# Kernel tuning notes

Hardware: AMD Instinct MI355X
Metric: run time of the kernel (lower is better)

## Reference

```python
import jax, jax.numpy as jnp
import numpy as np

NUM_HEADS = 32
MAX_BIAS_LENGTH = 1024
ROPE_BASE = 10000.0


def _rope_cos_sin(seq_len, head_dim, dtype):
    half = head_dim // 2
    inv_freq = 1.0 / (ROPE_BASE ** (jnp.arange(0, half, dtype=jnp.float32) / half))
    t = jnp.arange(seq_len, dtype=jnp.float32)
    freqs = jnp.outer(t, inv_freq)  # [S, half]
    return jnp.cos(freqs).astype(dtype), jnp.sin(freqs).astype(dtype)


def _apply_rope(x, cos, sin):
    # x: [B, S, H, D]; non-interleaved (GPT-NeoX / flash-attn style) rotary
    half = x.shape[-1] // 2
    x1, x2 = x[..., :half], x[..., half:]
    c = cos[None, :, None, :]
    s = sin[None, :, None, :]
    return jnp.concatenate([x1 * c - x2 * s, x1 * s + x2 * c], axis=-1)


def setup_inputs() -> dict:
    key = jax.random.key(0)
    ks = jax.random.split(key, 7)
    B, S, Dm = 2, 2048, 2048
    std = 1.0 / np.sqrt(Dm)
    return {
        "hidden_states": jax.random.normal(ks[0], (B, S, Dm), jnp.float32),
        "Wq": jax.random.normal(ks[1], (Dm, Dm), jnp.float32) * std,
        "Wk": jax.random.normal(ks[2], (Dm, Dm), jnp.float32) * std,
        "Wv": jax.random.normal(ks[3], (Dm, Dm), jnp.float32) * std,
        "Wo": jax.random.normal(ks[4], (Dm, Dm), jnp.float32) * std,
        "learnable_bias": jax.random.normal(ks[5], (NUM_HEADS, MAX_BIAS_LENGTH), jnp.float32) * 0.001,
        "softmax_offset": jnp.zeros((NUM_HEADS,), jnp.float32),
    }


def reference(hidden_states, Wq, Wk, Wv, Wo, learnable_bias, softmax_offset):
    B, S, Dm = hidden_states.shape
    H = NUM_HEADS
    D = Dm // H
    scale = D ** -0.5

    # projections (nn.Linear: x @ W.T)
    q = (hidden_states @ Wq.T).reshape(B, S, H, D)
    k = (hidden_states @ Wk.T).reshape(B, S, H, D)
    v = (hidden_states @ Wv.T).reshape(B, S, H, D)

    cos, sin = _rope_cos_sin(S, D, q.dtype)
    q = _apply_rope(q, cos, sin)
    k = _apply_rope(k, cos, sin)

    q = q.transpose(0, 2, 1, 3)  # [B, H, S, D]
    k = k.transpose(0, 2, 1, 3)
    v = v.transpose(0, 2, 1, 3)

    scores = jnp.einsum("bhid,bhjd->bhij", q, k) * scale  # [B, H, S, S]

    # per-diagonal learnable bias: diag = i - j in [0, MAX_BIAS_LENGTH)
    i = jnp.arange(S)[:, None]
    j = jnp.arange(S)[None, :]
    diag = i - j  # [S, S]
    causal = diag >= 0
    in_band = causal & (diag < MAX_BIAS_LENGTH)
    bias = jnp.where(in_band, learnable_bias[:, jnp.clip(diag, 0, MAX_BIAS_LENGTH - 1)], 0.0)  # [H, S, S]
    scores = scores + bias[None]
    scores = jnp.where(causal[None, None], scores, -jnp.inf)

    # softmax with learnable per-head offset (attention-sink logit)
    off = softmax_offset[None, :, None]  # [1, H, 1]
    m = jnp.maximum(jnp.max(scores, axis=-1), off)  # [B, H, S]
    p = jnp.exp(scores - m[..., None])
    denom = jnp.sum(p, axis=-1) + jnp.exp(off - m)  # [B, H, S]
    out = jnp.einsum("bhij,bhjd->bhid", p, v) / denom[..., None]

    out = out.transpose(0, 2, 1, 3).reshape(B, S, Dm)
    return out @ Wo.T
```

## Files before the change

kernel.cpp:

```cpp
#include <hip/hip_runtime.h>
#include <hip/hip_bf16.h>
#include <stdint.h>

typedef __bf16 bf16x8 __attribute__((ext_vector_type(8)));
typedef float f32x4 __attribute__((ext_vector_type(4)));
typedef unsigned short u16;
typedef u16 u16x4 __attribute__((ext_vector_type(4)));

#define S_LEN 2048
#define DMODEL 2048
#define NHEADS 32
#define BATCH 2
#define MROWS (BATCH * S_LEN)
#define BIAS_LEN 1024
#define LOG2E 1.44269504088896f

__device__ __forceinline__ u16 b16(float f) {
  union { __bf16 h; u16 u; } cv; cv.h = (__bf16)f; return cv.u;
}

__device__ __forceinline__ void gload16(const void* g, void* l) {
  __builtin_amdgcn_global_load_lds(
      (const __attribute__((address_space(1))) uint32_t*)g,
      (__attribute__((address_space(3))) uint32_t*)l, 16, 0, 0);
}

__global__ __launch_bounds__(256)
void cvt_bf16(const float* __restrict__ in, u16* __restrict__ out, int n) {
  int i = (blockIdx.x * 256 + threadIdx.x) * 4;
  if (i >= n) return;
  float4 v = *(const float4*)(in + i);
  u16x4 o = { b16(v.x), b16(v.y), b16(v.z), b16(v.w) };
  *(u16x4*)(out + i) = o;
}

__global__ __launch_bounds__(256)
void rope_tab(float* __restrict__ ct, float* __restrict__ st) {
  int idx = blockIdx.x * 256 + threadIdx.x;
  if (idx >= S_LEN * 32) return;
  int s = idx >> 5, d = idx & 31;
  float inv = exp2f((float)d * (-13.287712379549449f / 32.0f));
  float a = (float)s * inv;
  ct[idx] = cosf(a);
  st[idx] = sinf(a);
}

template<int EPI>
__global__ __launch_bounds__(256)
void gemm_bt(const u16* __restrict__ A, const u16* __restrict__ Bm,
             void* __restrict__ Cout,
             const float* __restrict__ ctab, const float* __restrict__ stab)
{
  __shared__ u16 sA[128 * 64];
  __shared__ u16 sB[128 * 64];
  const int tid  = threadIdx.x;
  const int lane = tid & 63;
  const int wid  = tid >> 6;
  const int wm   = wid >> 1, wn = wid & 1;
  const int lc   = lane & 15, lr = lane >> 4;
  const int tm   = blockIdx.y * 128;
  const int tn   = blockIdx.x * 128;

  f32x4 acc[4][4] = {};

  const u16* aS[4]; const u16* bS[4];
#pragma unroll
  for (int it = 0; it < 4; ++it) {
    int u = it * 256 + tid;
    int row = u >> 3;
    int ch  = (u & 7) ^ (row & 7);
    aS[it] = A  + (size_t)(tm + row) * DMODEL + ch * 8;
    bS[it] = Bm + (size_t)(tn + row) * DMODEL + ch * 8;
  }

  for (int k0 = 0; k0 < DMODEL; k0 += 64) {
    __syncthreads();
#pragma unroll
    for (int it = 0; it < 4; ++it) {
      int u = it * 256 + tid;
      gload16(aS[it] + k0, (char*)sA + u * 16);
      gload16(bS[it] + k0, (char*)sB + u * 16);
    }
    __syncthreads();
#pragma unroll
    for (int kk = 0; kk < 2; ++kk) {
      bf16x8 af[4], bq[4];
#pragma unroll
      for (int mi = 0; mi < 4; ++mi) {
        int row = wm * 64 + mi * 16 + lc;
        int ch  = (kk * 4 + lr) ^ (row & 7);
        af[mi] = *(const bf16x8*)((const char*)sA + row * 128 + ch * 16);
      }
#pragma unroll
      for (int ni = 0; ni < 4; ++ni) {
        int row = wn * 64 + ni * 16 + lc;
        int ch  = (kk * 4 + lr) ^ (row & 7);
        bq[ni] = *(const bf16x8*)((const char*)sB + row * 128 + ch * 16);
      }
#pragma unroll
      for (int mi = 0; mi < 4; ++mi)
#pragma unroll
        for (int ni = 0; ni < 4; ++ni)
          acc[mi][ni] = __builtin_amdgcn_mfma_f32_16x16x32_bf16(af[mi], bq[ni], acc[mi][ni], 0, 0, 0);
    }
  }

  if constexpr (EPI == 4) {
    float* C = (float*)Cout;
#pragma unroll
    for (int mi = 0; mi < 4; ++mi)
#pragma unroll
      for (int ni = 0; ni < 4; ++ni)
#pragma unroll
        for (int j = 0; j < 4; ++j) {
          int r = tm + wm * 64 + mi * 16 + lr * 4 + j;
          int c = tn + wn * 64 + ni * 16 + lc;
          C[(size_t)r * DMODEL + c] = acc[mi][ni][j];
        }
  } else if constexpr (EPI == 3) {
    u16* C = (u16*)Cout;
#pragma unroll
    for (int mi = 0; mi < 4; ++mi)
#pragma unroll
      for (int ni = 0; ni < 4; ++ni) {
        int col = tn + wn * 64 + ni * 16 + lc;
        int hh = col >> 6, d = col & 63;
        int m0 = tm + wm * 64 + mi * 16 + lr * 4;
        int bb = m0 >> 11, s = m0 & 2047;
        u16x4 v = { b16(acc[mi][ni][0]), b16(acc[mi][ni][1]),
                    b16(acc[mi][ni][2]), b16(acc[mi][ni][3]) };
        *(u16x4*)(C + (((size_t)bb * NHEADS + hh) * 64 + d) * S_LEN + s) = v;
      }
  } else {
    u16* C = (u16*)Cout;
#pragma unroll
    for (int mi = 0; mi < 4; ++mi)
#pragma unroll
      for (int ni = 0; ni < 2; ++ni)
#pragma unroll
        for (int j = 0; j < 4; ++j) {
          int col = tn + wn * 64 + ni * 16 + lc;
          int hh = col >> 6, dl = col & 63;
          int r = tm + wm * 64 + mi * 16 + lr * 4 + j;
          int bb = r >> 11, s = r & 2047;
          float x1 = acc[mi][ni][j], x2 = acc[mi][ni + 2][j];
          float cv = ctab[s * 32 + dl], sv = stab[s * 32 + dl];
          float o1 = x1 * cv - x2 * sv;
          float o2 = x1 * sv + x2 * cv;
          if constexpr (EPI == 1) {
            o1 *= 0.125f * LOG2E; o2 *= 0.125f * LOG2E;
          }
          size_t base = (((size_t)bb * NHEADS + hh) * S_LEN + s) * 64 + dl;
          C[base]      = b16(o1);
          C[base + 32] = b16(o2);
        }
  }
}

__global__ __launch_bounds__(512, 6)
void attn_kernel(const u16* __restrict__ Q, const u16* __restrict__ K,
                 const u16* __restrict__ V, const float* __restrict__ biasg,
                 const float* __restrict__ offg, u16* __restrict__ O)
{
  __shared__ __align__(16) u16 sK[2][64 * 64];
  __shared__ __align__(16) u16 sV[2][64 * 64];
  __shared__ __align__(16) u16 sP[8][16 * 40];
  __shared__ float sBias[BIAS_LEN];

  const int tid = threadIdx.x, lane = tid & 63, wid = tid >> 6;
  const int lc = lane & 15, lr = lane >> 4;

  const int L   = blockIdx.x;
  const int idx = L >> 3;
  const int pi  = idx >> 3;
  const int bh  = (L & 7) + 8 * (idx & 7);
  const int h  = bh & 31;
  const int b  = bh >> 5;
  const int qtA  = 31 - pi;
  const int myQt = (wid < 4) ? qtA : pi;
  const int qw   = myQt * 64 + (wid & 3) * 16;

  for (int i = tid; i < BIAS_LEN; i += 512) sBias[i] = biasg[h * BIAS_LEN + i] * LOG2E;
  const float off = offg[h] * LOG2E;

  const u16* qp = Q + ((size_t)bh * S_LEN + qw + lc) * 64;
  bf16x8 aq0 = *(const bf16x8*)(qp + lr * 8);
  bf16x8 aq1 = *(const bf16x8*)(qp + 32 + lr * 8);

  const int srow = tid >> 3;
  const int sch  = (tid & 7) ^ (srow & 7);
  const u16* kSrc = K + ((size_t)bh * S_LEN + srow) * 64 + sch * 8;
  const u16* vSrc = V + ((size_t)bh * 64 + srow) * S_LEN + sch * 8;

  float m = off, lsum = 1.0f;
  f32x4 o[4] = {};

  gload16(kSrc, (char*)sK[0] + tid * 16);
  gload16(vSrc, (char*)sV[0] + tid * 16);
  __syncthreads();

  for (int t = 0; t <= qtA; ++t) {
    const int cur = t & 1;
    if (t < qtA) {
      gload16(kSrc + (size_t)(t + 1) * 64 * 64, (char*)sK[cur ^ 1] + tid * 16);
      gload16(vSrc + (t + 1) * 64,              (char*)sV[cur ^ 1] + tid * 16);
    }

    if (t <= myQt) {
      const int kt = t * 64;
      f32x4 sc[4];
      __builtin_amdgcn_s_setprio(1);
#pragma unroll
      for (int f = 0; f < 4; ++f) {
        int row = f * 16 + lc;
        bf16x8 k0 = *(const bf16x8*)((const char*)sK[cur] + row * 128 + ((lr) ^ (row & 7)) * 16);
        bf16x8 k1 = *(const bf16x8*)((const char*)sK[cur] + row * 128 + ((4 + lr) ^ (row & 7)) * 16);
        f32x4 z = {};
        z     = __builtin_amdgcn_mfma_f32_16x16x32_bf16(k0, aq0, z, 0, 0, 0);
        sc[f] = __builtin_amdgcn_mfma_f32_16x16x32_bf16(k1, aq1, z, 0, 0, 0);
      }
      __builtin_amdgcn_s_setprio(0);

      const int db  = qw + lc - kt;
      const int dqt = qw - kt;
      float pvv[4][4];
      if (t == myQt) {
#pragma unroll
        for (int f = 0; f < 4; ++f)
#pragma unroll
          for (int j = 0; j < 4; ++j) {
            int dd = db - (f * 16 + lr * 4 + j);
            float bb = sBias[dd & 1023];
            pvv[f][j] = (dd >= 0) ? sc[f][j] + bb : -1e30f;
          }
      } else if (dqt <= 1008) {
#pragma unroll
        for (int f = 0; f < 4; ++f)
#pragma unroll
          for (int j = 0; j < 4; ++j)
            pvv[f][j] = sc[f][j] + sBias[db - (f * 16 + lr * 4 + j)];
      } else if (dqt < 1088) {
#pragma unroll
        for (int f = 0; f < 4; ++f)
#pragma unroll
          for (int j = 0; j < 4; ++j) {
            int dd = db - (f * 16 + lr * 4 + j);
            float bb = (dd < 1024) ? sBias[dd & 1023] : 0.0f;
            pvv[f][j] = sc[f][j] + bb;
          }
      } else {
#pragma unroll
        for (int f = 0; f < 4; ++f)
#pragma unroll
          for (int j = 0; j < 4; ++j)
            pvv[f][j] = sc[f][j];
      }

      float pmax = -1e30f;
#pragma unroll
      for (int f = 0; f < 4; ++f) {
        float a = fmaxf(fmaxf(pvv[f][0], pvv[f][1]), fmaxf(pvv[f][2], pvv[f][3]));
        pmax = fmaxf(pmax, a);
      }
      pmax = fmaxf(pmax, __shfl_xor(pmax, 16, 64));
      pmax = fmaxf(pmax, __shfl_xor(pmax, 32, 64));

      if (__any(pmax > m + 8.0f)) {
        float mn = fmaxf(m, pmax);
        float al = exp2f(m - mn);
        m = mn;
        lsum *= al;
        float aj[4];
#pragma unroll
        for (int j = 0; j < 4; ++j) aj[j] = __shfl(al, lr * 4 + j, 64);
#pragma unroll
        for (int f2 = 0; f2 < 4; ++f2)
#pragma unroll
          for (int j = 0; j < 4; ++j) o[f2][j] *= aj[j];
      }

      float rsum = 0.0f;
#pragma unroll
      for (int f = 0; f < 4; ++f)
#pragma unroll
        for (int j = 0; j < 4; ++j) {
          float p = exp2f(pvv[f][j] - m);
          pvv[f][j] = p;
          rsum += p;
        }
      rsum += __shfl_xor(rsum, 16, 64);
      rsum += __shfl_xor(rsum, 32, 64);
      lsum += rsum;

      u16* myP = sP[wid];
#pragma unroll
      for (int kk = 0; kk < 2; ++kk) {
#pragma unroll
        for (int fl = 0; fl < 2; ++fl) {
          int f = kk * 2 + fl;
          u16x4 w = { b16(pvv[f][0]), b16(pvv[f][1]), b16(pvv[f][2]), b16(pvv[f][3]) };
          *(u16x4*)(myP + lc * 40 + fl * 16 + lr * 4) = w;
        }
        asm volatile("s_waitcnt lgkmcnt(0)" ::: "memory");
        __builtin_amdgcn_sched_barrier(0);
        bf16x8 ap = *(const bf16x8*)(myP + lc * 40 + lr * 8);
        __builtin_amdgcn_s_setprio(1);
#pragma unroll
        for (int f2 = 0; f2 < 4; ++f2) {
          int drow = f2 * 16 + lc;
          int chh = (kk * 4 + lr) ^ (drow & 7);
          bf16x8 bv = *(const bf16x8*)((const char*)sV[cur] + drow * 128 + chh * 16);
          o[f2] = __builtin_amdgcn_mfma_f32_16x16x32_bf16(ap, bv, o[f2], 0, 0, 0);
        }
        __builtin_amdgcn_s_setprio(0);
      }
    }
    __syncthreads();
  }

  float ls[4];
#pragma unroll
  for (int j = 0; j < 4; ++j) ls[j] = __shfl(lsum, lr * 4 + j, 64);
#pragma unroll
  for (int f2 = 0; f2 < 4; ++f2)
#pragma unroll
    for (int j = 0; j < 4; ++j) {
      int i = qw + lr * 4 + j;
      int d = f2 * 16 + lc;
      size_t addr = (((size_t)(b * S_LEN + i)) * NHEADS + h) * 64 + d;
      O[addr] = b16(o[f2][j] / ls[j]);
    }
}

extern "C" void kernel_launch(void* const* d_in, const int* in_sizes, int n_in,
                              void* d_out, int out_size, void* d_ws, size_t ws_size,
                              hipStream_t stream)
{
  const float* hs   = (const float*)d_in[0];
  const float* Wq   = (const float*)d_in[1];
  const float* Wk   = (const float*)d_in[2];
  const float* Wv   = (const float*)d_in[3];
  const float* Wo   = (const float*)d_in[4];
  const float* bias = (const float*)d_in[5];
  const float* off  = (const float*)d_in[6];

  char* p = (char*)d_ws;
  u16* hs_b = (u16*)p; p += (size_t)MROWS * DMODEL * 2;
  u16* wq_b = (u16*)p; p += (size_t)DMODEL * DMODEL * 2;
  u16* wk_b = (u16*)p; p += (size_t)DMODEL * DMODEL * 2;
  u16* wv_b = (u16*)p; p += (size_t)DMODEL * DMODEL * 2;
  u16* wo_b = (u16*)p; p += (size_t)DMODEL * DMODEL * 2;
  u16* qf   = (u16*)p; p += (size_t)MROWS * DMODEL * 2;
  u16* kf   = (u16*)p; p += (size_t)MROWS * DMODEL * 2;
  u16* vt   = (u16*)p; p += (size_t)MROWS * DMODEL * 2;
  u16* att  = (u16*)p; p += (size_t)MROWS * DMODEL * 2;
  float* ct = (float*)p; p += (size_t)S_LEN * 32 * 4;
  float* st = (float*)p; p += (size_t)S_LEN * 32 * 4;
  (void)ws_size; (void)in_sizes; (void)n_in; (void)out_size;

  cvt_bf16<<<(MROWS * DMODEL) / 1024, 256, 0, stream>>>(hs, hs_b, MROWS * DMODEL);
  cvt_bf16<<<(DMODEL * DMODEL) / 1024, 256, 0, stream>>>(Wq, wq_b, DMODEL * DMODEL);
  cvt_bf16<<<(DMODEL * DMODEL) / 1024, 256, 0, stream>>>(Wk, wk_b, DMODEL * DMODEL);
  cvt_bf16<<<(DMODEL * DMODEL) / 1024, 256, 0, stream>>>(Wv, wv_b, DMODEL * DMODEL);
  cvt_bf16<<<(DMODEL * DMODEL) / 1024, 256, 0, stream>>>(Wo, wo_b, DMODEL * DMODEL);
  rope_tab<<<(S_LEN * 32) / 256, 256, 0, stream>>>(ct, st);

  dim3 g(DMODEL / 128, MROWS / 128);
  gemm_bt<1><<<g, 256, 0, stream>>>(hs_b, wq_b, qf, ct, st);
  gemm_bt<2><<<g, 256, 0, stream>>>(hs_b, wk_b, kf, ct, st);
  gemm_bt<3><<<g, 256, 0, stream>>>(hs_b, wv_b, vt, nullptr, nullptr);
  attn_kernel<<<dim3(16 * 64), 512, 0, stream>>>(qf, kf, vt, bias, off, att);
  gemm_bt<4><<<g, 256, 0, stream>>>(att, wo_b, d_out, nullptr, nullptr);
}
```

Before: 304.2 us.

## Split paired-tile attention blocks into one-qtile 256-thread blocks with bf16 bias

Each attention block previously handled two query tiles (heavy and light paired) with 512 threads. Now each 256-thread block handles one query tile, launched heaviest-first across twice as many blocks. The bias table is pre-converted to bf16 and scaled by log2e in a new small kernel, which halves its LDS footprint. LDS offsets are precomputed and the final divide becomes a reciprocal multiply. This trades the old balanced pairing for dynamic scheduling, and the bias loses precision from the bf16 rounding.

```diff
diff --git a/kernel.cpp b/kernel.cpp
--- a/kernel.cpp
+++ b/kernel.cpp
@@ -43,6 +43,12 @@
   float a = (float)s * inv;
   ct[idx] = cosf(a);
   st[idx] = sinf(a);
+}
+
+__global__ __launch_bounds__(256)
+void bias_prep(const float* __restrict__ in, u16* __restrict__ out) {
+  int i = blockIdx.x * 256 + threadIdx.x;
+  out[i] = b16(in[i] * LOG2E);
 }
 
 template<int EPI>
@@ -157,170 +163,191 @@
   }
 }
 
-__global__ __launch_bounds__(512, 6)
+__global__ __launch_bounds__(256, 4)
 void attn_kernel(const u16* __restrict__ Q, const u16* __restrict__ K,
-                 const u16* __restrict__ V, const float* __restrict__ biasg,
+                 const u16* __restrict__ V, const u16* __restrict__ bias16,
                  const float* __restrict__ offg, u16* __restrict__ O)
 {
   __shared__ __align__(16) u16 sK[2][64 * 64];
   __shared__ __align__(16) u16 sV[2][64 * 64];
-  __shared__ __align__(16) u16 sP[8][16 * 40];
-  __shared__ float sBias[BIAS_LEN];
+  __shared__ __align__(16) u16 sP[4][16 * 40];
+  __shared__ __align__(8)  u16 sBias[BIAS_LEN];
 
   const int tid = threadIdx.x, lane = tid & 63, wid = tid >> 6;
   const int lc = lane & 15, lr = lane >> 4;
-
-  const int L   = blockIdx.x;
-  const int idx = L >> 3;
-  const int pi  = idx >> 3;
-  const int bh  = (L & 7) + 8 * (idx & 7);
+  const int L  = blockIdx.x;
+  const int qt = 31 - (L >> 6);
+  const int bh = L & 63;
   const int h  = bh & 31;
   const int b  = bh >> 5;
-  const int qtA  = 31 - pi;
-  const int myQt = (wid < 4) ? qtA : pi;
-  const int qw   = myQt * 64 + (wid & 3) * 16;
-
-  for (int i = tid; i < BIAS_LEN; i += 512) sBias[i] = biasg[h * BIAS_LEN + i] * LOG2E;
+  const int qw = qt * 64 + wid * 16;
+
+  *(u16x4*)&sBias[tid * 4] = *(const u16x4*)&bias16[h * BIAS_LEN + tid * 4];
   const float off = offg[h] * LOG2E;
 
   const u16* qp = Q + ((size_t)bh * S_LEN + qw + lc) * 64;
   bf16x8 aq0 = *(const bf16x8*)(qp + lr * 8);
   bf16x8 aq1 = *(const bf16x8*)(qp + 32 + lr * 8);
 
-  const int srow = tid >> 3;
-  const int sch  = (tid & 7) ^ (srow & 7);
-  const u16* kSrc = K + ((size_t)bh * S_LEN + srow) * 64 + sch * 8;
-  const u16* vSrc = V + ((size_t)bh * 64 + srow) * S_LEN + sch * 8;
+  const u16* kS[2]; const u16* vS[2];
+#pragma unroll
+  for (int it = 0; it < 2; ++it) {
+    int u = it * 256 + tid;
+    int row = u >> 3;
+    int ch  = (u & 7) ^ (row & 7);
+    kS[it] = K + ((size_t)bh * S_LEN + row) * 64 + ch * 8;
+    vS[it] = V + ((size_t)bh * 64 + row) * S_LEN + ch * 8;
+  }
+
+  int offK[4][2], offV[2][4];
+#pragma unroll
+  for (int f = 0; f < 4; ++f) {
+    int row = f * 16 + lc;
+    offK[f][0] = row * 128 + ((lr) ^ (row & 7)) * 16;
+    offK[f][1] = row * 128 + ((4 + lr) ^ (row & 7)) * 16;
+  }
+#pragma unroll
+  for (int kk = 0; kk < 2; ++kk)
+#pragma unroll
+    for (int f2 = 0; f2 < 4; ++f2) {
+      int drow = f2 * 16 + lc;
+      offV[kk][f2] = drow * 128 + ((kk * 4 + lr) ^ (drow & 7)) * 16;
+    }
 
   float m = off, lsum = 1.0f;
   f32x4 o[4] = {};
 
-  gload16(kSrc, (char*)sK[0] + tid * 16);
-  gload16(vSrc, (char*)sV[0] + tid * 16);
+#pragma unroll
+  for (int it = 0; it < 2; ++it) {
+    int u = it * 256 + tid;
+    gload16(kS[it], (char*)sK[0] + u * 16);
+    gload16(vS[it], (char*)sV[0] + u * 16);
+  }
   __syncthreads();
 
-  for (int t = 0; t <= qtA; ++t) {
+  for (int t = 0; t <= qt; ++t) {
     const int cur = t & 1;
-    if (t < qtA) {
-      gload16(kSrc + (size_t)(t + 1) * 64 * 64, (char*)sK[cur ^ 1] + tid * 16);
-      gload16(vSrc + (t + 1) * 64,              (char*)sV[cur ^ 1] + tid * 16);
-    }
-
-    if (t <= myQt) {
-      const int kt = t * 64;
-      f32x4 sc[4];
+    if (t < qt) {
+#pragma unroll
+      for (int it = 0; it < 2; ++it) {
+        int u = it * 256 + tid;
+        gload16(kS[it] + (size_t)(t + 1) * 4096, (char*)sK[cur ^ 1] + u * 16);
+        gload16(vS[it] + (t + 1) * 64,           (char*)sV[cur ^ 1] + u * 16);
+      }
+    }
+
+    const int kt = t * 64;
+    f32x4 sc[4];
+    __builtin_amdgcn_s_setprio(1);
+#pragma unroll
+    for (int f = 0; f < 4; ++f) {
+      bf16x8 k0 = *(const bf16x8*)((const char*)sK[cur] + offK[f][0]);
+      bf16x8 k1 = *(const bf16x8*)((const char*)sK[cur] + offK[f][1]);
+      f32x4 z = {};
+      z     = __builtin_amdgcn_mfma_f32_16x16x32_bf16(k0, aq0, z, 0, 0, 0);
+      sc[f] = __builtin_amdgcn_mfma_f32_16x16x32_bf16(k1, aq1, z, 0, 0, 0);
+    }
+    __builtin_amdgcn_s_setprio(0);
+
+    const int db  = qw + lc - kt;
+    const int dqt = qw - kt;
+    float pvv[4][4];
+    if (t == qt) {
+#pragma unroll
+      for (int f = 0; f < 4; ++f)
+#pragma unroll
+        for (int j = 0; j < 4; ++j) {
+          int dd = db - (f * 16 + lr * 4 + j);
+          float bb = __uint_as_float((uint32_t)sBias[dd & 1023] << 16);
+          pvv[f][j] = (dd >= 0) ? sc[f][j] + bb : -1e30f;
+        }
+    } else if (dqt <= 1008) {
+#pragma unroll
+      for (int f = 0; f < 4; ++f)
+#pragma unroll
+        for (int j = 0; j < 4; ++j) {
+          float bb = __uint_as_float((uint32_t)sBias[db - (f * 16 + lr * 4 + j)] << 16);
+          pvv[f][j] = sc[f][j] + bb;
+        }
+    } else if (dqt < 1088) {
+#pragma unroll
+      for (int f = 0; f < 4; ++f)
+#pragma unroll
+        for (int j = 0; j < 4; ++j) {
+          int dd = db - (f * 16 + lr * 4 + j);
+          float bb = (dd < 1024) ? __uint_as_float((uint32_t)sBias[dd & 1023] << 16) : 0.0f;
+          pvv[f][j] = sc[f][j] + bb;
+        }
+    } else {
+#pragma unroll
+      for (int f = 0; f < 4; ++f)
+#pragma unroll
+        for (int j = 0; j < 4; ++j)
+          pvv[f][j] = sc[f][j];
+    }
+
+    float pmax = -1e30f;
+#pragma unroll
+    for (int f = 0; f < 4; ++f) {
+      float a = fmaxf(fmaxf(pvv[f][0], pvv[f][1]), fmaxf(pvv[f][2], pvv[f][3]));
+      pmax = fmaxf(pmax, a);
+    }
+    pmax = fmaxf(pmax, __shfl_xor(pmax, 16, 64));
+    pmax = fmaxf(pmax, __shfl_xor(pmax, 32, 64));
+
+    if (__any(pmax > m + 8.0f)) {
+      float mn = fmaxf(m, pmax);
+      float al = exp2f(m - mn);
+      m = mn;
+      lsum *= al;
+      float aj[4];
+#pragma unroll
+      for (int j = 0; j < 4; ++j) aj[j] = __shfl(al, lr * 4 + j, 64);
+#pragma unroll
+      for (int f2 = 0; f2 < 4; ++f2)
+#pragma unroll
+        for (int j = 0; j < 4; ++j) o[f2][j] *= aj[j];
+    }
+
+    float rsum = 0.0f;
+#pragma unroll
+    for (int f = 0; f < 4; ++f)
+#pragma unroll
+      for (int j = 0; j < 4; ++j) {
+        float p = exp2f(pvv[f][j] - m);
+        pvv[f][j] = p;
+        rsum += p;
+      }
+    rsum += __shfl_xor(rsum, 16, 64);
+    rsum += __shfl_xor(rsum, 32, 64);
+    lsum += rsum;
+
+    u16* myP = sP[wid];
+#pragma unroll
+    for (int kk = 0; kk < 2; ++kk) {
+#pragma unroll
+      for (int fl = 0; fl < 2; ++fl) {
+        int f = kk * 2 + fl;
+        u16x4 w = { b16(pvv[f][0]), b16(pvv[f][1]), b16(pvv[f][2]), b16(pvv[f][3]) };
+        *(u16x4*)(myP + lc * 40 + fl * 16 + lr * 4) = w;
+      }
+      asm volatile("s_waitcnt lgkmcnt(0)" ::: "memory");
+      __builtin_amdgcn_sched_barrier(0);
+      bf16x8 ap = *(const bf16x8*)(myP + lc * 40 + lr * 8);
       __builtin_amdgcn_s_setprio(1);
 #pragma unroll
-      for (int f = 0; f < 4; ++f) {
-        int row = f * 16 + lc;
-        bf16x8 k0 = *(const bf16x8*)((const char*)sK[cur] + row * 128 + ((lr) ^ (row & 7)) * 16);
-        bf16x8 k1 = *(const bf16x8*)((const char*)sK[cur] + row * 128 + ((4 + lr) ^ (row & 7)) * 16);
-        f32x4 z = {};
-        z     = __builtin_amdgcn_mfma_f32_16x16x32_bf16(k0, aq0, z, 0, 0, 0);
-        sc[f] = __builtin_amdgcn_mfma_f32_16x16x32_bf16(k1, aq1, z, 0, 0, 0);
+      for (int f2 = 0; f2 < 4; ++f2) {
+        bf16x8 bv = *(const bf16x8*)((const char*)sV[cur] + offV[kk][f2]);
+        o[f2] = __builtin_amdgcn_mfma_f32_16x16x32_bf16(ap, bv, o[f2], 0, 0, 0);
       }
       __builtin_amdgcn_s_setprio(0);
-
-      const int db  = qw + lc - kt;
-      const int dqt = qw - kt;
-      float pvv[4][4];
-      if (t == myQt) {
-#pragma unroll
-        for (int f = 0; f < 4; ++f)
-#pragma unroll
-          for (int j = 0; j < 4; ++j) {
-            int dd = db - (f * 16 + lr * 4 + j);
-            float bb = sBias[dd & 1023];
-            pvv[f][j] = (dd >= 0) ? sc[f][j] + bb : -1e30f;
-          }
-      } else if (dqt <= 1008) {
-#pragma unroll
-        for (int f = 0; f < 4; ++f)
-#pragma unroll
-          for (int j = 0; j < 4; ++j)
-            pvv[f][j] = sc[f][j] + sBias[db - (f * 16 + lr * 4 + j)];
-      } else if (dqt < 1088) {
-#pragma unroll
-        for (int f = 0; f < 4; ++f)
-#pragma unroll
-          for (int j = 0; j < 4; ++j) {
-            int dd = db - (f * 16 + lr * 4 + j);
-            float bb = (dd < 1024) ? sBias[dd & 1023] : 0.0f;
-            pvv[f][j] = sc[f][j] + bb;
-          }
-      } else {
-#pragma unroll
-        for (int f = 0; f < 4; ++f)
-#pragma unroll
-          for (int j = 0; j < 4; ++j)
-            pvv[f][j] = sc[f][j];
-      }
-
-      float pmax = -1e30f;
-#pragma unroll
-      for (int f = 0; f < 4; ++f) {
-        float a = fmaxf(fmaxf(pvv[f][0], pvv[f][1]), fmaxf(pvv[f][2], pvv[f][3]));
-        pmax = fmaxf(pmax, a);
-      }
-      pmax = fmaxf(pmax, __shfl_xor(pmax, 16, 64));
-      pmax = fmaxf(pmax, __shfl_xor(pmax, 32, 64));
-
-      if (__any(pmax > m + 8.0f)) {
-        float mn = fmaxf(m, pmax);
-        float al = exp2f(m - mn);
-        m = mn;
-        lsum *= al;
-        float aj[4];
-#pragma unroll
-        for (int j = 0; j < 4; ++j) aj[j] = __shfl(al, lr * 4 + j, 64);
-#pragma unroll
-        for (int f2 = 0; f2 < 4; ++f2)
-#pragma unroll
-          for (int j = 0; j < 4; ++j) o[f2][j] *= aj[j];
-      }
-
-      float rsum = 0.0f;
-#pragma unroll
-      for (int f = 0; f < 4; ++f)
-#pragma unroll
-        for (int j = 0; j < 4; ++j) {
-          float p = exp2f(pvv[f][j] - m);
-          pvv[f][j] = p;
-          rsum += p;
-        }
-      rsum += __shfl_xor(rsum, 16, 64);
-      rsum += __shfl_xor(rsum, 32, 64);
-      lsum += rsum;
-
-      u16* myP = sP[wid];
-#pragma unroll
-      for (int kk = 0; kk < 2; ++kk) {
-#pragma unroll
-        for (int fl = 0; fl < 2; ++fl) {
-          int f = kk * 2 + fl;
-          u16x4 w = { b16(pvv[f][0]), b16(pvv[f][1]), b16(pvv[f][2]), b16(pvv[f][3]) };
-          *(u16x4*)(myP + lc * 40 + fl * 16 + lr * 4) = w;
-        }
-        asm volatile("s_waitcnt lgkmcnt(0)" ::: "memory");
-        __builtin_amdgcn_sched_barrier(0);
-        bf16x8 ap = *(const bf16x8*)(myP + lc * 40 + lr * 8);
-        __builtin_amdgcn_s_setprio(1);
-#pragma unroll
-        for (int f2 = 0; f2 < 4; ++f2) {
-          int drow = f2 * 16 + lc;
-          int chh = (kk * 4 + lr) ^ (drow & 7);
-          bf16x8 bv = *(const bf16x8*)((const char*)sV[cur] + drow * 128 + chh * 16);
-          o[f2] = __builtin_amdgcn_mfma_f32_16x16x32_bf16(ap, bv, o[f2], 0, 0, 0);
-        }
-        __builtin_amdgcn_s_setprio(0);
-      }
     }
     __syncthreads();
   }
 
   float ls[4];
 #pragma unroll
-  for (int j = 0; j < 4; ++j) ls[j] = __shfl(lsum, lr * 4 + j, 64);
+  for (int j = 0; j < 4; ++j) ls[j] = 1.0f / __shfl(lsum, lr * 4 + j, 64);
 #pragma unroll
   for (int f2 = 0; f2 < 4; ++f2)
 #pragma unroll
@@ -328,7 +355,7 @@
       int i = qw + lr * 4 + j;
       int d = f2 * 16 + lc;
       size_t addr = (((size_t)(b * S_LEN + i)) * NHEADS + h) * 64 + d;
-      O[addr] = b16(o[f2][j] / ls[j]);
+      O[addr] = b16(o[f2][j] * ls[j]);
     }
 }
 
@@ -356,6 +383,7 @@
   u16* att  = (u16*)p; p += (size_t)MROWS * DMODEL * 2;
   float* ct = (float*)p; p += (size_t)S_LEN * 32 * 4;
   float* st = (float*)p; p += (size_t)S_LEN * 32 * 4;
+  u16* b16t = (u16*)p; p += (size_t)NHEADS * BIAS_LEN * 2;
   (void)ws_size; (void)in_sizes; (void)n_in; (void)out_size;
 
   cvt_bf16<<<(MROWS * DMODEL) / 1024, 256, 0, stream>>>(hs, hs_b, MROWS * DMODEL);
@@ -364,11 +392,12 @@
   cvt_bf16<<<(DMODEL * DMODEL) / 1024, 256, 0, stream>>>(Wv, wv_b, DMODEL * DMODEL);
   cvt_bf16<<<(DMODEL * DMODEL) / 1024, 256, 0, stream>>>(Wo, wo_b, DMODEL * DMODEL);
   rope_tab<<<(S_LEN * 32) / 256, 256, 0, stream>>>(ct, st);
+  bias_prep<<<(NHEADS * BIAS_LEN) / 256, 256, 0, stream>>>(bias, b16t);
 
   dim3 g(DMODEL / 128, MROWS / 128);
   gemm_bt<1><<<g, 256, 0, stream>>>(hs_b, wq_b, qf, ct, st);
   gemm_bt<2><<<g, 256, 0, stream>>>(hs_b, wk_b, kf, ct, st);
   gemm_bt<3><<<g, 256, 0, stream>>>(hs_b, wv_b, vt, nullptr, nullptr);
-  attn_kernel<<<dim3(16 * 64), 512, 0, stream>>>(qf, kf, vt, bias, off, att);
+  attn_kernel<<<dim3(32 * 64), 256, 0, stream>>>(qf, kf, vt, b16t, off, att);
   gemm_bt<4><<<g, 256, 0, stream>>>(att, wo_b, d_out, nullptr, nullptr);
 }
```

Result: slower. 326.8 us (+7.4%).
